# Kernel optimization log

Hardware: AMD Instinct MI355X
Metric: run time of the kernel (lower is better)

The kernel has to match this reference:

```python
import jax, jax.numpy as jnp
import numpy as np

N_NODES = 50000
N_EDGES = 800000
IN_CH = 128
OUT_CH = 64
H1, C1 = 8, 8            # conv1: heads=8, out=8, concat -> 64
H2, C2 = 1, OUT_CH       # conv2: heads=1, out=64, concat=False
NEG_SLOPE = 0.2


def gat_conv(x, src, dst, W, att_src, att_dst, bias, heads, ch, concat):
    """PyG GATConv (self loops assumed already appended to src/dst).
    x: [N, F_in], W: [F_in, heads*ch], att_*: [heads, ch], bias: [heads*ch] or [ch]."""
    N = x.shape[0]
    h = (x @ W).reshape(N, heads, ch)                       # [N,H,C]
    a_s = jnp.einsum('nhc,hc->nh', h, att_src)              # [N,H]
    a_d = jnp.einsum('nhc,hc->nh', h, att_dst)              # [N,H]
    e = jax.nn.leaky_relu(a_s[src] + a_d[dst], NEG_SLOPE)   # [E,H]
    # segment softmax over incoming edges of each destination node
    m = jax.ops.segment_max(e, dst, num_segments=N)         # [N,H]
    ex = jnp.exp(e - m[dst])
    s = jax.ops.segment_sum(ex, dst, num_segments=N)        # [N,H]
    alpha = ex / (s[dst] + 1e-16)                           # [E,H]
    out = jax.ops.segment_sum(h[src] * alpha[:, :, None], dst, num_segments=N)  # [N,H,C]
    out = out.reshape(N, heads * ch) if concat else out.mean(axis=1)
    return out + bias


def setup_inputs() -> dict:
    key = jax.random.key(0)
    ks = jax.random.split(key, 12)
    glorot = lambda k, shape: jax.random.normal(k, shape, jnp.float32) * np.sqrt(2.0 / (shape[0] + shape[-1]))
    x = jax.random.normal(ks[0], (N_NODES, IN_CH), jnp.float32)
    edge_index = jax.random.randint(ks[1], (2, N_EDGES), 0, N_NODES, jnp.int64 if jax.config.read('jax_enable_x64') else jnp.int32).astype(jnp.int32)
    W1 = glorot(ks[2], (IN_CH, H1 * C1))
    att_src1 = glorot(ks[3], (H1, C1))
    att_dst1 = glorot(ks[4], (H1, C1))
    b1 = jnp.zeros((H1 * C1,), jnp.float32)
    W2 = glorot(ks[5], (H1 * C1, H2 * C2))
    att_src2 = glorot(ks[6], (H2, C2))
    att_dst2 = glorot(ks[7], (H2, C2))
    b2 = jnp.zeros((C2,), jnp.float32)
    return {"x": x, "edge_index": edge_index, "W1": W1, "att_src1": att_src1,
            "att_dst1": att_dst1, "b1": b1, "W2": W2, "att_src2": att_src2,
            "att_dst2": att_dst2, "b2": b2}


def reference(x, edge_index, W1, att_src1, att_dst1, b1, W2, att_src2, att_dst2, b2):
    N = x.shape[0]
    loops = jnp.arange(N, dtype=edge_index.dtype)
    src = jnp.concatenate([edge_index[0], loops])  # add_self_loops=True (PyG default)
    dst = jnp.concatenate([edge_index[1], loops])
    h = gat_conv(x, src, dst, W1, att_src1, att_dst1, b1, H1, C1, concat=True)
    h = jax.nn.elu(h)
    # F.dropout(training=self.training): identity in eval mode
    out = gat_conv(h, src, dst, W2, att_src2, att_dst2, b2, H2, C2, concat=False)
    return out
```

## Files before the change

kernel.cpp:

```cpp
#include <hip/hip_runtime.h>

#define NN 50000
#define NE 800000
#define NEG_SLOPE 0.2f
#define CAP 64

__device__ __forceinline__ float lrelu(float v) { return v > 0.f ? v : NEG_SLOPE * v; }
__device__ __forceinline__ unsigned short f2bf(float f) {
    unsigned u = __float_as_uint(f);
    return (unsigned short)((u + 0x7FFFu + ((u >> 16) & 1u)) >> 16);
}
__device__ __forceinline__ float rlane(float v, int l) {
    return __int_as_float(__builtin_amdgcn_readlane(__float_as_int(v), l));
}

__global__ __launch_bounds__(256) void setup(const float* __restrict__ W1,
                                             const float* __restrict__ W2,
                                             const float* __restrict__ as2,
                                             const float* __restrict__ ad2,
                                             int4* __restrict__ cnt4,
                                             float* __restrict__ W1S,
                                             float* __restrict__ W2S,
                                             float* __restrict__ w_as2,
                                             float* __restrict__ w_ad2) {
    int gid = blockIdx.x * 256 + threadIdx.x;
    if (gid < 12500) cnt4[gid] = make_int4(0, 0, 0, 0);
    if (gid < 8192) {
        int k = gid >> 6, c = gid & 63;
        W1S[((k >> 2) * 64 + c) * 4 + (k & 3)] = W1[k * 64 + c];
    } else if (gid < 12288) {
        int t = gid - 8192;
        int k = t >> 6, c = t & 63;
        W2S[((k >> 2) * 64 + c) * 4 + (k & 3)] = W2[k * 64 + c];
    }
    if (gid < 64) {
        float s = 0.f;
        for (int c = 0; c < 64; ++c) s += W2[gid * 64 + c] * as2[c];
        w_as2[gid] = s;
    } else if (gid < 128) {
        int k = gid - 64;
        float s = 0.f;
        for (int c = 0; c < 64; ++c) s += W2[k * 64 + c] * ad2[c];
        w_ad2[k] = s;
    }
}

__global__ __launch_bounds__(256) void build_gemm1(const int* __restrict__ ei,
                                                   int* __restrict__ cnt,
                                                   int* __restrict__ bucket,
                                                   const float* __restrict__ x,
                                                   const float* __restrict__ W1S,
                                                   const float* __restrict__ att_s,
                                                   const float* __restrict__ att_d,
                                                   unsigned short* __restrict__ h1b,
                                                   float* __restrict__ a_s,
                                                   float2* __restrict__ nd1) {
    if (blockIdx.x < 3125) {
        int e = blockIdx.x * 256 + threadIdx.x;
        int d = ei[NE + e];
        int pos = atomicAdd(&cnt[d], 1) & (CAP - 1);
        bucket[d * CAP + pos] = ei[e];
        return;
    }
    int lane = threadIdx.x & 63;
    int wv   = __builtin_amdgcn_readfirstlane(threadIdx.x >> 6);
    int n0   = (blockIdx.x - 3125) * 16 + wv * 4;
    const float* __restrict__ xr = x + (size_t)n0 * 128;
    const float4* __restrict__ wp = (const float4*)W1S;
    float4 acc = {0.f, 0.f, 0.f, 0.f};
#pragma unroll 4
    for (int k4 = 0; k4 < 32; ++k4) {
        float4 w = wp[k4 * 64 + lane];
        const float* xk = xr + k4 * 4;
        acc.x += xk[0]   * w.x + xk[1]   * w.y + xk[2]   * w.z + xk[3]   * w.w;
        acc.y += xk[128] * w.x + xk[129] * w.y + xk[130] * w.z + xk[131] * w.w;
        acc.z += xk[256] * w.x + xk[257] * w.y + xk[258] * w.z + xk[259] * w.w;
        acc.w += xk[384] * w.x + xk[385] * w.y + xk[386] * w.z + xk[387] * w.w;
    }
    float as_l = att_s[lane], ad_l = att_d[lane];
    float av[4] = {acc.x, acc.y, acc.z, acc.w};
#pragma unroll
    for (int r = 0; r < 4; ++r) {
        float a = av[r];
        h1b[(size_t)(n0 + r) * 64 + lane] = f2bf(a);
        float ps = a * as_l, pd = a * ad_l;
        ps += __shfl_xor(ps, 1, 64); pd += __shfl_xor(pd, 1, 64);
        ps += __shfl_xor(ps, 2, 64); pd += __shfl_xor(pd, 2, 64);
        ps += __shfl_xor(ps, 4, 64); pd += __shfl_xor(pd, 4, 64);
        if ((lane & 7) == 0) {
            int h = lane >> 3;
            a_s[(n0 + r) * 8 + h] = ps;
            nd1[(n0 + r) * 8 + h] = make_float2(pd, lrelu(ps + pd));
        }
    }
}

__global__ __launch_bounds__(256) void agg1(const int* __restrict__ bucket,
                                            const int* __restrict__ cnt,
                                            const float* __restrict__ a_s,
                                            const float2* __restrict__ nd1,
                                            const unsigned short* __restrict__ h1b,
                                            const float* __restrict__ b1,
                                            const float* __restrict__ w_as2,
                                            const float* __restrict__ w_ad2,
                                            unsigned short* __restrict__ xhb,
                                            float* __restrict__ a_s2,
                                            float2* __restrict__ nd2) {
    int wv   = threadIdx.x >> 6;
    int lane = threadIdx.x & 63;
    int d    = blockIdx.x * 4 + wv;
    int base = d * CAP;
    int dg   = min(cnt[d], CAP);
    int sub  = lane >> 3, hch = lane & 7;
    float2 nd = nd1[d * 8 + hch];
    float acc0 = 0.f, acc1 = 0.f, acc2 = 0.f, acc3 = 0.f;
    float acc4 = 0.f, acc5 = 0.f, acc6 = 0.f, acc7 = 0.f;
    float sm = 0.f;
    int k = sub;
    int s0 = 0, s1 = 0;
    float as0 = 0.f;
    uint4 hv0 = make_uint4(0, 0, 0, 0);
    if (k < dg)     s0 = bucket[base + k];
    if (k + 8 < dg) s1 = bucket[base + k + 8];
    if (k < dg) {
        as0 = a_s[s0 * 8 + hch];
        hv0 = *(const uint4*)&h1b[(size_t)s0 * 64 + hch * 8];
    }
    for (; k < dg; k += 8) {
        int   s2  = (k + 16 < dg) ? bucket[base + k + 16] : 0;
        float as1 = 0.f;
        uint4 hv1 = make_uint4(0, 0, 0, 0);
        if (k + 8 < dg) {
            as1 = a_s[s1 * 8 + hch];
            hv1 = *(const uint4*)&h1b[(size_t)s1 * 64 + hch * 8];
        }
        float ex = __expf(lrelu(as0 + nd.x) - nd.y);
        acc0 += __uint_as_float(hv0.x << 16)          * ex;
        acc1 += __uint_as_float(hv0.x & 0xffff0000u)  * ex;
        acc2 += __uint_as_float(hv0.y << 16)          * ex;
        acc3 += __uint_as_float(hv0.y & 0xffff0000u)  * ex;
        acc4 += __uint_as_float(hv0.z << 16)          * ex;
        acc5 += __uint_as_float(hv0.z & 0xffff0000u)  * ex;
        acc6 += __uint_as_float(hv0.w << 16)          * ex;
        acc7 += __uint_as_float(hv0.w & 0xffff0000u)  * ex;
        sm += ex;
        s0 = s1; s1 = s2; as0 = as1; hv0 = hv1;
    }
    if (sub == 0) {
        uint4 hv = *(const uint4*)&h1b[(size_t)d * 64 + hch * 8];
        acc0 += __uint_as_float(hv.x << 16);
        acc1 += __uint_as_float(hv.x & 0xffff0000u);
        acc2 += __uint_as_float(hv.y << 16);
        acc3 += __uint_as_float(hv.y & 0xffff0000u);
        acc4 += __uint_as_float(hv.z << 16);
        acc5 += __uint_as_float(hv.z & 0xffff0000u);
        acc6 += __uint_as_float(hv.w << 16);
        acc7 += __uint_as_float(hv.w & 0xffff0000u);
        sm += 1.f;
    }
#pragma unroll
    for (int m = 8; m < 64; m <<= 1) {
        acc0 += __shfl_xor(acc0, m, 64); acc1 += __shfl_xor(acc1, m, 64);
        acc2 += __shfl_xor(acc2, m, 64); acc3 += __shfl_xor(acc3, m, 64);
        acc4 += __shfl_xor(acc4, m, 64); acc5 += __shfl_xor(acc5, m, 64);
        acc6 += __shfl_xor(acc6, m, 64); acc7 += __shfl_xor(acc7, m, 64);
        sm   += __shfl_xor(sm, m, 64);
    }
    float inv = 1.f / sm;
    int li = (lane & 7) * 8;
    float4 bl = *(const float4*)&b1[li];
    float4 bh = *(const float4*)&b1[li + 4];
    float4 lo, hi;
    lo.x = acc0 * inv + bl.x; lo.x = lo.x > 0.f ? lo.x : expm1f(lo.x);
    lo.y = acc1 * inv + bl.y; lo.y = lo.y > 0.f ? lo.y : expm1f(lo.y);
    lo.z = acc2 * inv + bl.z; lo.z = lo.z > 0.f ? lo.z : expm1f(lo.z);
    lo.w = acc3 * inv + bl.w; lo.w = lo.w > 0.f ? lo.w : expm1f(lo.w);
    hi.x = acc4 * inv + bh.x; hi.x = hi.x > 0.f ? hi.x : expm1f(hi.x);
    hi.y = acc5 * inv + bh.y; hi.y = hi.y > 0.f ? hi.y : expm1f(hi.y);
    hi.z = acc6 * inv + bh.z; hi.z = hi.z > 0.f ? hi.z : expm1f(hi.z);
    hi.w = acc7 * inv + bh.w; hi.w = hi.w > 0.f ? hi.w : expm1f(hi.w);
    if (lane < 8) {
        uint4 pk;
        pk.x = ((unsigned)f2bf(lo.y) << 16) | f2bf(lo.x);
        pk.y = ((unsigned)f2bf(lo.w) << 16) | f2bf(lo.z);
        pk.z = ((unsigned)f2bf(hi.y) << 16) | f2bf(hi.x);
        pk.w = ((unsigned)f2bf(hi.w) << 16) | f2bf(hi.z);
        *(uint4*)&xhb[(size_t)d * 64 + lane * 8] = pk;
    }
    float4 s0v = *(const float4*)&w_as2[li], s1v = *(const float4*)&w_as2[li + 4];
    float4 d0v = *(const float4*)&w_ad2[li], d1v = *(const float4*)&w_ad2[li + 4];
    float ps = lo.x*s0v.x + lo.y*s0v.y + lo.z*s0v.z + lo.w*s0v.w
             + hi.x*s1v.x + hi.y*s1v.y + hi.z*s1v.z + hi.w*s1v.w;
    float pd = lo.x*d0v.x + lo.y*d0v.y + lo.z*d0v.z + lo.w*d0v.w
             + hi.x*d1v.x + hi.y*d1v.y + hi.z*d1v.z + hi.w*d1v.w;
    ps += __shfl_xor(ps, 1, 64); pd += __shfl_xor(pd, 1, 64);
    ps += __shfl_xor(ps, 2, 64); pd += __shfl_xor(pd, 2, 64);
    ps += __shfl_xor(ps, 4, 64); pd += __shfl_xor(pd, 4, 64);
    if (lane == 0) {
        a_s2[d] = ps;
        nd2[d]  = make_float2(pd, lrelu(ps + pd));
    }
}

__global__ __launch_bounds__(256) void agg2(const int* __restrict__ bucket,
                                            const int* __restrict__ cnt,
                                            const float* __restrict__ a_s2,
                                            const float2* __restrict__ nd2,
                                            const unsigned short* __restrict__ xhb,
                                            const float* __restrict__ W2S,
                                            const float* __restrict__ b2,
                                            float* __restrict__ out) {
    int wv   = threadIdx.x >> 6;
    int lane = threadIdx.x & 63;
    int d    = blockIdx.x * 4 + wv;
    int base = d * CAP;
    int dg   = min(cnt[d], CAP);
    int sub  = lane >> 3, hch = lane & 7;
    float2 nd = nd2[d];
    float acc0 = 0.f, acc1 = 0.f, acc2 = 0.f, acc3 = 0.f;
    float acc4 = 0.f, acc5 = 0.f, acc6 = 0.f, acc7 = 0.f;
    float sm = 0.f;
    int k = sub;
    int s0 = 0, s1 = 0;
    float as0 = 0.f;
    uint4 hv0 = make_uint4(0, 0, 0, 0);
    if (k < dg)     s0 = bucket[base + k];
    if (k + 8 < dg) s1 = bucket[base + k + 8];
    if (k < dg) {
        as0 = a_s2[s0];
        hv0 = *(const uint4*)&xhb[(size_t)s0 * 64 + hch * 8];
    }
    for (; k < dg; k += 8) {
        int   s2  = (k + 16 < dg) ? bucket[base + k + 16] : 0;
        float as1 = 0.f;
        uint4 hv1 = make_uint4(0, 0, 0, 0);
        if (k + 8 < dg) {
            as1 = a_s2[s1];
            hv1 = *(const uint4*)&xhb[(size_t)s1 * 64 + hch * 8];
        }
        float ex = __expf(lrelu(as0 + nd.x) - nd.y);
        acc0 += __uint_as_float(hv0.x << 16)          * ex;
        acc1 += __uint_as_float(hv0.x & 0xffff0000u)  * ex;
        acc2 += __uint_as_float(hv0.y << 16)          * ex;
        acc3 += __uint_as_float(hv0.y & 0xffff0000u)  * ex;
        acc4 += __uint_as_float(hv0.z << 16)          * ex;
        acc5 += __uint_as_float(hv0.z & 0xffff0000u)  * ex;
        acc6 += __uint_as_float(hv0.w << 16)          * ex;
        acc7 += __uint_as_float(hv0.w & 0xffff0000u)  * ex;
        sm += ex;
        s0 = s1; s1 = s2; as0 = as1; hv0 = hv1;
    }
    if (sub == 0) {
        uint4 hv = *(const uint4*)&xhb[(size_t)d * 64 + hch * 8];
        acc0 += __uint_as_float(hv.x << 16);
        acc1 += __uint_as_float(hv.x & 0xffff0000u);
        acc2 += __uint_as_float(hv.y << 16);
        acc3 += __uint_as_float(hv.y & 0xffff0000u);
        acc4 += __uint_as_float(hv.z << 16);
        acc5 += __uint_as_float(hv.z & 0xffff0000u);
        acc6 += __uint_as_float(hv.w << 16);
        acc7 += __uint_as_float(hv.w & 0xffff0000u);
        sm += 1.f;
    }
#pragma unroll
    for (int m = 8; m < 64; m <<= 1) {
        acc0 += __shfl_xor(acc0, m, 64); acc1 += __shfl_xor(acc1, m, 64);
        acc2 += __shfl_xor(acc2, m, 64); acc3 += __shfl_xor(acc3, m, 64);
        acc4 += __shfl_xor(acc4, m, 64); acc5 += __shfl_xor(acc5, m, 64);
        acc6 += __shfl_xor(acc6, m, 64); acc7 += __shfl_xor(acc7, m, 64);
        sm   += __shfl_xor(sm, m, 64);
    }
    float inv = 1.f / sm;
    float t0 = acc0 * inv, t1 = acc1 * inv, t2 = acc2 * inv, t3 = acc3 * inv;
    float t4 = acc4 * inv, t5 = acc5 * inv, t6 = acc6 * inv, t7 = acc7 * inv;
    const float4* wp = (const float4*)W2S;
    float o = 0.f;
#pragma unroll
    for (int k4 = 0; k4 < 16; ++k4) {
        float4 w = wp[k4 * 64 + lane];
        int j = k4 >> 1;
        if (k4 & 1)
            o += rlane(t4, j) * w.x + rlane(t5, j) * w.y + rlane(t6, j) * w.z + rlane(t7, j) * w.w;
        else
            o += rlane(t0, j) * w.x + rlane(t1, j) * w.y + rlane(t2, j) * w.z + rlane(t3, j) * w.w;
    }
    out[(size_t)d * 64 + lane] = o + b2[lane];
}

extern "C" void kernel_launch(void* const* d_in, const int* in_sizes, int n_in,
                              void* d_out, int out_size, void* d_ws, size_t ws_size,
                              hipStream_t stream) {
    const float* x   = (const float*)d_in[0];
    const int*   ei  = (const int*)d_in[1];
    const float* W1  = (const float*)d_in[2];
    const float* as1 = (const float*)d_in[3];
    const float* ad1 = (const float*)d_in[4];
    const float* b1  = (const float*)d_in[5];
    const float* W2  = (const float*)d_in[6];
    const float* as2 = (const float*)d_in[7];
    const float* ad2 = (const float*)d_in[8];
    const float* b2  = (const float*)d_in[9];
    float* out = (float*)d_out;

    float* ws = (float*)d_ws;
    unsigned short* h1b = (unsigned short*)ws;
    unsigned short* xhb = (unsigned short*)(ws + 1600000);
    float*  a_s1 = ws + 3200000;
    float2* nd1  = (float2*)(ws + 3600000);
    float*  a_s2 = ws + 4400000;
    float2* nd2  = (float2*)(ws + 4450000);
    int* cnt     = (int*)(ws + 4550000);
    int* bucket  = cnt + 50000;
    float* W1S   = (float*)(bucket + 3200000);
    float* W2S   = W1S + 8192;
    float* w_as2 = W2S + 4096;
    float* w_ad2 = w_as2 + 64;

    setup<<<49, 256, 0, stream>>>(W1, W2, as2, ad2, (int4*)cnt, W1S, W2S, w_as2, w_ad2);
    build_gemm1<<<6250, 256, 0, stream>>>(ei, cnt, bucket, x, W1S, as1, ad1,
                                          h1b, a_s1, nd1);
    agg1<<<12500, 256, 0, stream>>>(bucket, cnt, a_s1, nd1, h1b, b1,
                                    w_as2, w_ad2, xhb, a_s2, nd2);
    agg2<<<12500, 256, 0, stream>>>(bucket, cnt, a_s2, nd2, xhb, W2S, b2, out);
}
```

Baseline: 171.1 us.

## Store adjacency buckets as 16-bit indices and batch four edges per thread

Source indices in the per-destination buckets are stored as unsigned shorts, since node ids stay below 65536. This halves the bucket traffic written during the build and read by both aggregation kernels. The build phase now gives each thread four edges, issuing their loads and atomics together for more memory-level parallelism with fewer blocks. In agg2 the softmax normalization is applied once to the projected output instead of to eight accumulators before the readlane GEMV. The 16-bit encoding silently breaks if the node count ever exceeds 65535.

```diff
diff --git a/kernel.cpp b/kernel.cpp
--- a/kernel.cpp
+++ b/kernel.cpp
@@ -3,6 +3,7 @@
 #define NN 50000
 #define NE 800000
 #define NEG_SLOPE 0.2f
+#define S4 200192
 #define CAP 64
 
 __device__ __forceinline__ float lrelu(float v) { return v > 0.f ? v : NEG_SLOPE * v; }
@@ -47,7 +48,7 @@
 
 __global__ __launch_bounds__(256) void build_gemm1(const int* __restrict__ ei,
                                                    int* __restrict__ cnt,
-                                                   int* __restrict__ bucket,
+                                                   unsigned short* __restrict__ bucket,
                                                    const float* __restrict__ x,
                                                    const float* __restrict__ W1S,
                                                    const float* __restrict__ att_s,
@@ -55,16 +56,28 @@
                                                    unsigned short* __restrict__ h1b,
                                                    float* __restrict__ a_s,
                                                    float2* __restrict__ nd1) {
-    if (blockIdx.x < 3125) {
-        int e = blockIdx.x * 256 + threadIdx.x;
-        int d = ei[NE + e];
-        int pos = atomicAdd(&cnt[d], 1) & (CAP - 1);
-        bucket[d * CAP + pos] = ei[e];
+    if (blockIdx.x < 782) {
+        int tid = blockIdx.x * 256 + threadIdx.x;
+        int e0 = tid, e1 = tid + S4, e2 = tid + 2 * S4, e3 = tid + 3 * S4;
+        bool p3 = e3 < NE;
+        int s0 = ei[e0], d0 = ei[NE + e0];
+        int s1 = ei[e1], d1 = ei[NE + e1];
+        int s2 = ei[e2], d2 = ei[NE + e2];
+        int s3 = 0, d3 = 0;
+        if (p3) { s3 = ei[e3]; d3 = ei[NE + e3]; }
+        int r0 = atomicAdd(&cnt[d0], 1) & (CAP - 1);
+        int r1 = atomicAdd(&cnt[d1], 1) & (CAP - 1);
+        int r2 = atomicAdd(&cnt[d2], 1) & (CAP - 1);
+        int r3 = p3 ? (atomicAdd(&cnt[d3], 1) & (CAP - 1)) : 0;
+        bucket[(d0 << 6) + r0] = (unsigned short)s0;
+        bucket[(d1 << 6) + r1] = (unsigned short)s1;
+        bucket[(d2 << 6) + r2] = (unsigned short)s2;
+        if (p3) bucket[(d3 << 6) + r3] = (unsigned short)s3;
         return;
     }
     int lane = threadIdx.x & 63;
     int wv   = __builtin_amdgcn_readfirstlane(threadIdx.x >> 6);
-    int n0   = (blockIdx.x - 3125) * 16 + wv * 4;
+    int n0   = (blockIdx.x - 782) * 16 + wv * 4;
     const float* __restrict__ xr = x + (size_t)n0 * 128;
     const float4* __restrict__ wp = (const float4*)W1S;
     float4 acc = {0.f, 0.f, 0.f, 0.f};
@@ -95,7 +108,7 @@
     }
 }
 
-__global__ __launch_bounds__(256) void agg1(const int* __restrict__ bucket,
+__global__ __launch_bounds__(256) void agg1(const unsigned short* __restrict__ bucket,
                                             const int* __restrict__ cnt,
                                             const float* __restrict__ a_s,
                                             const float2* __restrict__ nd1,
@@ -109,7 +122,7 @@
     int wv   = threadIdx.x >> 6;
     int lane = threadIdx.x & 63;
     int d    = blockIdx.x * 4 + wv;
-    int base = d * CAP;
+    int base = d << 6;
     int dg   = min(cnt[d], CAP);
     int sub  = lane >> 3, hch = lane & 7;
     float2 nd = nd1[d * 8 + hch];
@@ -127,7 +140,7 @@
         hv0 = *(const uint4*)&h1b[(size_t)s0 * 64 + hch * 8];
     }
     for (; k < dg; k += 8) {
-        int   s2  = (k + 16 < dg) ? bucket[base + k + 16] : 0;
+        int   s2  = (k + 16 < dg) ? (int)bucket[base + k + 16] : 0;
         float as1 = 0.f;
         uint4 hv1 = make_uint4(0, 0, 0, 0);
         if (k + 8 < dg) {
@@ -202,7 +215,7 @@
     }
 }
 
-__global__ __launch_bounds__(256) void agg2(const int* __restrict__ bucket,
+__global__ __launch_bounds__(256) void agg2(const unsigned short* __restrict__ bucket,
                                             const int* __restrict__ cnt,
                                             const float* __restrict__ a_s2,
                                             const float2* __restrict__ nd2,
@@ -213,7 +226,7 @@
     int wv   = threadIdx.x >> 6;
     int lane = threadIdx.x & 63;
     int d    = blockIdx.x * 4 + wv;
-    int base = d * CAP;
+    int base = d << 6;
     int dg   = min(cnt[d], CAP);
     int sub  = lane >> 3, hch = lane & 7;
     float2 nd = nd2[d];
@@ -231,7 +244,7 @@
         hv0 = *(const uint4*)&xhb[(size_t)s0 * 64 + hch * 8];
     }
     for (; k < dg; k += 8) {
-        int   s2  = (k + 16 < dg) ? bucket[base + k + 16] : 0;
+        int   s2  = (k + 16 < dg) ? (int)bucket[base + k + 16] : 0;
         float as1 = 0.f;
         uint4 hv1 = make_uint4(0, 0, 0, 0);
         if (k + 8 < dg) {
@@ -271,8 +284,6 @@
         sm   += __shfl_xor(sm, m, 64);
     }
     float inv = 1.f / sm;
-    float t0 = acc0 * inv, t1 = acc1 * inv, t2 = acc2 * inv, t3 = acc3 * inv;
-    float t4 = acc4 * inv, t5 = acc5 * inv, t6 = acc6 * inv, t7 = acc7 * inv;
     const float4* wp = (const float4*)W2S;
     float o = 0.f;
 #pragma unroll
@@ -280,11 +291,11 @@
         float4 w = wp[k4 * 64 + lane];
         int j = k4 >> 1;
         if (k4 & 1)
-            o += rlane(t4, j) * w.x + rlane(t5, j) * w.y + rlane(t6, j) * w.z + rlane(t7, j) * w.w;
+            o += rlane(acc4, j) * w.x + rlane(acc5, j) * w.y + rlane(acc6, j) * w.z + rlane(acc7, j) * w.w;
         else
-            o += rlane(t0, j) * w.x + rlane(t1, j) * w.y + rlane(t2, j) * w.z + rlane(t3, j) * w.w;
-    }
-    out[(size_t)d * 64 + lane] = o + b2[lane];
+            o += rlane(acc0, j) * w.x + rlane(acc1, j) * w.y + rlane(acc2, j) * w.z + rlane(acc3, j) * w.w;
+    }
+    out[(size_t)d * 64 + lane] = o * inv + b2[lane];
 }
 
 extern "C" void kernel_launch(void* const* d_in, const int* in_sizes, int n_in,
@@ -310,14 +321,14 @@
     float*  a_s2 = ws + 4400000;
     float2* nd2  = (float2*)(ws + 4450000);
     int* cnt     = (int*)(ws + 4550000);
-    int* bucket  = cnt + 50000;
+    unsigned short* bucket = (unsigned short*)(cnt + 50000);
     float* W1S   = (float*)(bucket + 3200000);
     float* W2S   = W1S + 8192;
     float* w_as2 = W2S + 4096;
     float* w_ad2 = w_as2 + 64;
 
     setup<<<49, 256, 0, stream>>>(W1, W2, as2, ad2, (int4*)cnt, W1S, W2S, w_as2, w_ad2);
-    build_gemm1<<<6250, 256, 0, stream>>>(ei, cnt, bucket, x, W1S, as1, ad1,
+    build_gemm1<<<3907, 256, 0, stream>>>(ei, cnt, bucket, x, W1S, as1, ad1,
                                           h1b, a_s1, nd1);
     agg1<<<12500, 256, 0, stream>>>(bucket, cnt, a_s1, nd1, h1b, b1,
                                     w_as2, w_ad2, xhb, a_s2, nd2);
```

Result: faster. 159.6 us (-6.7%).
